# Kernel tuning notes

Measured on AMD Instinct MI355X. Metric: run time of the kernel, lower is better.

## Reference

```python
import jax, jax.numpy as jnp
import numpy as np

DIM = 1024
NUM_HEADS = 16
HEAD_DIM = DIM // NUM_HEADS


def setup_inputs() -> dict:
    key = jax.random.key(0)
    ks = jax.random.split(key, 9)
    B, T, D = 4, 8192, DIM
    s = 1.0 / np.sqrt(D)
    return {
        "x": jax.random.normal(ks[0], (B, T, D), dtype=jnp.float32),
        "Wq": jax.random.normal(ks[1], (D, D), dtype=jnp.float32) * s,
        "bq": jnp.zeros((D,), dtype=jnp.float32),
        "Wk": jax.random.normal(ks[2], (D, D), dtype=jnp.float32) * s,
        "bk": jnp.zeros((D,), dtype=jnp.float32),
        "Wv": jax.random.normal(ks[3], (D, D), dtype=jnp.float32) * s,
        "bv": jnp.zeros((D,), dtype=jnp.float32),
        "Wo": jax.random.normal(ks[4], (D, D), dtype=jnp.float32) * s,
        "bo": jnp.zeros((D,), dtype=jnp.float32),
    }


def _feature_map(x):
    # elu(x) + 1
    return jax.nn.elu(x) + 1.0


def reference(x, Wq, bq, Wk, bk, Wv, bv, Wo, bo):
    B, T, D = x.shape
    H, hd = NUM_HEADS, HEAD_DIM
    q = (x @ Wq.T + bq).reshape(B, T, H, hd)
    k = (x @ Wk.T + bk).reshape(B, T, H, hd)
    v = (x @ Wv.T + bv).reshape(B, T, H, hd)
    q = _feature_map(q)
    k = _feature_map(k)
    eps = 1e-6
    kv = jnp.einsum('bthd,bthm->bhmd', k, v)      # [B,H,hd,hd]
    k_sum = k.sum(axis=1)                          # [B,H,hd]
    z = 1.0 / (jnp.einsum('bthd,bhd->bth', q, k_sum) + eps)
    out = jnp.einsum('bthd,bhmd->bthm', q, kv) * z[..., None]
    out = out.reshape(B, T, D)
    return out @ Wo.T + bo
```

## Files before the change

kernel.cpp:

```cpp
#include <hip/hip_runtime.h>
#include <stdint.h>

typedef __bf16 bf16x8 __attribute__((ext_vector_type(8)));
typedef float f32x4 __attribute__((ext_vector_type(4)));
typedef unsigned short u16x8 __attribute__((ext_vector_type(8)));
typedef unsigned short u16x4 __attribute__((ext_vector_type(4)));

#define MFMA16(a, b, c) __builtin_amdgcn_mfma_f32_16x16x32_bf16(a, b, c, 0, 0, 0)

#define TSEQ 8192
#define BATCH 4
#define MROWS (BATCH * TSEQ)

static __device__ __forceinline__ unsigned short f2bf(float f) {
  union { float f; unsigned u; } v; v.f = f;
  unsigned u = v.u + 0x7FFFu + ((v.u >> 16) & 1u);
  return (unsigned short)(u >> 16);
}
static __device__ __forceinline__ float bf2f(unsigned short h) {
  union { unsigned u; float f; } v; v.u = ((unsigned)h) << 16; return v.f;
}
static __device__ __forceinline__ void gload16(const void* g, void* l) {
  __builtin_amdgcn_global_load_lds((const __attribute__((address_space(1))) void*)g,
                                   (__attribute__((address_space(3))) void*)l, 16, 0, 0);
}

__global__ __launch_bounds__(256) void cvt_bf16(const float* __restrict__ s,
                                                unsigned short* __restrict__ d, int n) {
  int i = (blockIdx.x * 256 + threadIdx.x) * 8;
  if (i >= n) return;
  const float4 a = *(const float4*)(s + i);
  const float4 b = *(const float4*)(s + i + 4);
  u16x8 o;
  o[0] = f2bf(a.x); o[1] = f2bf(a.y); o[2] = f2bf(a.z); o[3] = f2bf(a.w);
  o[4] = f2bf(b.x); o[5] = f2bf(b.y); o[6] = f2bf(b.z); o[7] = f2bf(b.w);
  *(u16x8*)(d + i) = o;
}

static __device__ __forceinline__ void gemm_core(const unsigned short* __restrict__ A,
                                                 const unsigned short* __restrict__ B,
                                                 int rowA0, int rowB0,
                                                 char* As, char* Bs, f32x4 acc[4][4]) {
  const int tid = threadIdx.x;
  const int l = tid & 63, w = tid >> 6;
  const int wr = (w >> 1) * 64, wc = (w & 1) * 64;
  for (int kk = 0; kk < 1024; kk += 32) {
    #pragma unroll
    for (int r2 = 0; r2 < 2; ++r2) {
      const int ci = r2 * 256 + tid;
      const int row = ci >> 2;
      const int csrc = (ci & 3) ^ ((row >> 1) & 3);
      char* la = As + (r2 * 256 + w * 64) * 16;
      gload16(A + (size_t)(rowA0 + row) * 1024 + kk + csrc * 8, la);
      char* lb = Bs + (r2 * 256 + w * 64) * 16;
      gload16(B + (size_t)(rowB0 + row) * 1024 + kk + csrc * 8, lb);
    }
    __syncthreads();
    bf16x8 af[4], bfr[4];
    #pragma unroll
    for (int m = 0; m < 4; ++m) {
      const int r = wr + m * 16 + (l & 15);
      const int c = (l >> 4) ^ ((r >> 1) & 3);
      af[m] = *(const bf16x8*)(As + r * 64 + c * 16);
      const int rb = wc + m * 16 + (l & 15);
      const int cb = (l >> 4) ^ ((rb >> 1) & 3);
      bfr[m] = *(const bf16x8*)(Bs + rb * 64 + cb * 16);
    }
    #pragma unroll
    for (int m = 0; m < 4; ++m)
      #pragma unroll
      for (int n = 0; n < 4; ++n)
        acc[m][n] = MFMA16(af[m], bfr[n], acc[m][n]);
    __syncthreads();
  }
}

__global__ __launch_bounds__(256) void qkv_gemm(const unsigned short* __restrict__ xbf,
                                                const unsigned short* __restrict__ wcat,
                                                const float* __restrict__ bq,
                                                const float* __restrict__ bk,
                                                const float* __restrict__ bv,
                                                unsigned short* __restrict__ qout,
                                                unsigned short* __restrict__ kout,
                                                unsigned short* __restrict__ vout) {
  __shared__ char As[8192];
  __shared__ char Bs[8192];
  f32x4 acc[4][4] = {};
  const int bx = blockIdx.x, by = blockIdx.y;
  gemm_core(xbf, wcat, by * 128, bx * 128, As, Bs, acc);

  const int region = bx >> 3;
  const float* bias = (region == 0) ? bq : (region == 1) ? bk : bv;
  unsigned short* dst = (region == 0) ? qout : (region == 1) ? kout : vout;
  const int l = threadIdx.x & 63, w = threadIdx.x >> 6;
  const int wr = (w >> 1) * 64, wc = (w & 1) * 64;
  const int colbase = (bx & 7) * 128 + wc;
  #pragma unroll
  for (int m = 0; m < 4; ++m) {
    #pragma unroll
    for (int n = 0; n < 4; ++n) {
      const int col = colbase + n * 16 + (l & 15);
      const float bb = bias[col];
      #pragma unroll
      for (int j = 0; j < 4; ++j) {
        const int row = by * 128 + wr + m * 16 + (l >> 4) * 4 + j;
        float v = acc[m][n][j] + bb;
        if (region < 2) v = (v > 0.f) ? (v + 1.f) : __expf(v);
        dst[(size_t)row * 1024 + col] = f2bf(v);
      }
    }
  }
}

__global__ __launch_bounds__(64) void kv_reduce(const unsigned short* __restrict__ kbf,
                                                const unsigned short* __restrict__ vbf,
                                                float* __restrict__ part) {
  const int bh = blockIdx.x, tc = blockIdx.y;
  const int b = bh >> 4, h = bh & 15;
  const int l = threadIdx.x;
  const int tm = l & 15, td = l >> 4;
  const unsigned short* kb = kbf + (size_t)b * TSEQ * 1024 + h * 64;
  const unsigned short* vb = vbf + (size_t)b * TSEQ * 1024 + h * 64;
  float acc[4][16] = {};
  float ksum = 0.f;
  const int t0 = tc * 256;
  #pragma unroll 2
  for (int t = t0; t < t0 + 256; ++t) {
    const unsigned short* krow = kb + (size_t)t * 1024;
    const unsigned short* vrow = vb + (size_t)t * 1024;
    const u16x8 k8a = *(const u16x8*)(krow + td * 16);
    const u16x8 k8b = *(const u16x8*)(krow + td * 16 + 8);
    const u16x4 v4 = *(const u16x4*)(vrow + tm * 4);
    float kf[16];
    #pragma unroll
    for (int j = 0; j < 8; ++j) { kf[j] = bf2f(k8a[j]); kf[8 + j] = bf2f(k8b[j]); }
    float vf[4];
    #pragma unroll
    for (int i = 0; i < 4; ++i) vf[i] = bf2f(v4[i]);
    ksum += bf2f(krow[td * 16 + tm]);
    #pragma unroll
    for (int i = 0; i < 4; ++i)
      #pragma unroll
      for (int j = 0; j < 16; ++j)
        acc[i][j] += vf[i] * kf[j];
  }
  float* ps = part + (size_t)(tc * 64 + bh) * 65 * 64;
  #pragma unroll
  for (int i = 0; i < 4; ++i) {
    const int m = tm * 4 + i;
    #pragma unroll
    for (int j = 0; j < 16; j += 4) {
      float4 o = make_float4(acc[i][j], acc[i][j + 1], acc[i][j + 2], acc[i][j + 3]);
      *(float4*)(ps + m * 64 + td * 16 + j) = o;
    }
  }
  ps[64 * 64 + td * 16 + tm] = ksum;
}

__global__ __launch_bounds__(256) void kv_finalize(const float* __restrict__ part,
                                                   unsigned short* __restrict__ bmat) {
  const int e = blockIdx.x * 256 + threadIdx.x;
  if (e >= 64 * 80 * 64) return;
  const int d = e & 63;
  const int r = (e >> 6) % 80;
  const int bh = e / (80 * 64);
  float s = 0.f;
  if (r < 65) {
    #pragma unroll
    for (int tc = 0; tc < 32; ++tc)
      s += part[((size_t)(tc * 64 + bh) * 65 + r) * 64 + d];
  }
  bmat[e] = f2bf(s);
}

__global__ __launch_bounds__(256) void attn_gemm(const unsigned short* __restrict__ qbf,
                                                 const unsigned short* __restrict__ bmat,
                                                 unsigned short* __restrict__ attn) {
  __shared__ char Qs[16384];
  __shared__ char Bs2[10240];
  const int bh = blockIdx.x, mt = blockIdx.y;
  const int b = bh >> 4, h = bh & 15;
  const int tid = threadIdx.x, l = tid & 63, w = tid >> 6;

  const unsigned short* qbase = qbf + (size_t)(b * TSEQ + mt * 128) * 1024 + h * 64;
  #pragma unroll
  for (int r4 = 0; r4 < 4; ++r4) {
    const int ci = r4 * 256 + tid;
    const int row = ci >> 3;
    const int csrc = (ci & 7) ^ (row & 7);
    gload16(qbase + (size_t)row * 1024 + csrc * 8, Qs + (r4 * 256 + w * 64) * 16);
  }
  const unsigned short* bbase = bmat + (size_t)bh * 80 * 64;
  #pragma unroll
  for (int r4 = 0; r4 < 3; ++r4) {
    const int ci = r4 * 256 + tid;
    if (ci < 640) {
      const int row = ci >> 3;
      const int csrc = (ci & 7) ^ (row & 7);
      gload16(bbase + row * 64 + csrc * 8, Bs2 + (r4 * 256 + w * 64) * 16);
    }
  }
  __syncthreads();

  f32x4 acc[2][5] = {};
  #pragma unroll
  for (int ks = 0; ks < 2; ++ks) {
    bf16x8 af[2], bfr[5];
    #pragma unroll
    for (int m = 0; m < 2; ++m) {
      const int r = w * 32 + m * 16 + (l & 15);
      const int c = ((l >> 4) + ks * 4) ^ (r & 7);
      af[m] = *(const bf16x8*)(Qs + r * 128 + c * 16);
    }
    #pragma unroll
    for (int n = 0; n < 5; ++n) {
      const int r = n * 16 + (l & 15);
      const int c = ((l >> 4) + ks * 4) ^ (r & 7);
      bfr[n] = *(const bf16x8*)(Bs2 + r * 128 + c * 16);
    }
    #pragma unroll
    for (int m = 0; m < 2; ++m)
      #pragma unroll
      for (int n = 0; n < 5; ++n)
        acc[m][n] = MFMA16(af[m], bfr[n], acc[m][n]);
  }

  unsigned short* arow = attn + (size_t)(b * TSEQ + mt * 128) * 1024 + h * 64;
  #pragma unroll
  for (int m = 0; m < 2; ++m) {
    #pragma unroll
    for (int j = 0; j < 4; ++j) {
      const float den = __shfl(acc[m][4][j], (l & 48));
      const float z = 1.f / (den + 1e-6f);
      const int row = w * 32 + m * 16 + (l >> 4) * 4 + j;
      #pragma unroll
      for (int n = 0; n < 4; ++n)
        arow[(size_t)row * 1024 + n * 16 + (l & 15)] = f2bf(acc[m][n][j] * z);
    }
  }
}

__global__ __launch_bounds__(256) void o_gemm(const unsigned short* __restrict__ attn,
                                              const unsigned short* __restrict__ wo,
                                              const float* __restrict__ bo,
                                              float* __restrict__ out) {
  __shared__ char As[8192];
  __shared__ char Bs[8192];
  f32x4 acc[4][4] = {};
  const int bx = blockIdx.x, by = blockIdx.y;
  gemm_core(attn, wo, by * 128, bx * 128, As, Bs, acc);
  const int l = threadIdx.x & 63, w = threadIdx.x >> 6;
  const int wr = (w >> 1) * 64, wc = (w & 1) * 64;
  #pragma unroll
  for (int m = 0; m < 4; ++m) {
    #pragma unroll
    for (int n = 0; n < 4; ++n) {
      const int col = bx * 128 + wc + n * 16 + (l & 15);
      const float bb = bo[col];
      #pragma unroll
      for (int j = 0; j < 4; ++j) {
        const int row = by * 128 + wr + m * 16 + (l >> 4) * 4 + j;
        out[(size_t)row * 1024 + col] = acc[m][n][j] + bb;
      }
    }
  }
}

extern "C" void kernel_launch(void* const* d_in, const int* in_sizes, int n_in,
                              void* d_out, int out_size, void* d_ws, size_t ws_size,
                              hipStream_t stream) {
  const float* x  = (const float*)d_in[0];
  const float* Wq = (const float*)d_in[1];
  const float* bq = (const float*)d_in[2];
  const float* Wk = (const float*)d_in[3];
  const float* bk = (const float*)d_in[4];
  const float* Wv = (const float*)d_in[5];
  const float* bv = (const float*)d_in[6];
  const float* Wo = (const float*)d_in[7];
  const float* bo = (const float*)d_in[8];
  float* out = (float*)d_out;
  char* ws = (char*)d_ws;

  unsigned short* xbf  = (unsigned short*)(ws + 0);
  unsigned short* wcat = (unsigned short*)(ws + 67108864);
  unsigned short* wobf = (unsigned short*)(ws + 73400320);
  unsigned short* qbf  = (unsigned short*)(ws + 75497472);
  unsigned short* kbf  = (unsigned short*)(ws + 142606336);
  unsigned short* vbf  = (unsigned short*)(ws + 209715200);
  float* part          = (float*)(ws + 0);
  unsigned short* bmat = (unsigned short*)(ws + 34078720);
  unsigned short* attn = kbf;

  cvt_bf16<<<16384, 256, 0, stream>>>(x, xbf, 33554432);
  cvt_bf16<<<512, 256, 0, stream>>>(Wq, wcat, 1048576);
  cvt_bf16<<<512, 256, 0, stream>>>(Wk, wcat + 1048576, 1048576);
  cvt_bf16<<<512, 256, 0, stream>>>(Wv, wcat + 2097152, 1048576);
  cvt_bf16<<<512, 256, 0, stream>>>(Wo, wobf, 1048576);

  qkv_gemm<<<dim3(24, 256), 256, 0, stream>>>(xbf, wcat, bq, bk, bv, qbf, kbf, vbf);
  kv_reduce<<<dim3(64, 32), 64, 0, stream>>>(kbf, vbf, part);
  kv_finalize<<<1280, 256, 0, stream>>>(part, bmat);
  attn_gemm<<<dim3(64, 64), 256, 0, stream>>>(qbf, bmat, attn);
  o_gemm<<<dim3(8, 256), 256, 0, stream>>>(attn, wobf, bo, out);
}
```

Measured before the change: 766.8 us.

## Replace QKV and output GEMMs with 256x256-tile pipelined 8-wave kernels

Both large projection GEMMs move from 128x128 tiles with a single-buffered LDS loop to 256x256 tiles on 512 threads. The new loop double-buffers A and B in LDS, issues global-to-LDS loads for the next k-slice while MFMAs run, and uses explicit waitcnt, barriers and setprio to interleave loads with compute. A swizzled block order improves L2 reuse across tiles. The larger tiles raise arithmetic intensity per byte loaded, at the cost of more registers and LDS per block, and the hand-written wait/barrier schedule is easy to get subtly wrong.

```diff
diff --git a/kernel.cpp b/kernel.cpp
--- a/kernel.cpp
+++ b/kernel.cpp
@@ -7,10 +7,14 @@
 typedef unsigned short u16x4 __attribute__((ext_vector_type(4)));
 
 #define MFMA16(a, b, c) __builtin_amdgcn_mfma_f32_16x16x32_bf16(a, b, c, 0, 0, 0)
+#define BAR() __builtin_amdgcn_s_barrier()
+#define LGK0() do { asm volatile("s_waitcnt lgkmcnt(0)" ::: "memory"); \
+                    __builtin_amdgcn_sched_barrier(0); } while (0)
+#define VMC(n) asm volatile("s_waitcnt vmcnt(" #n ")" ::: "memory")
+#define PRIO(p) __builtin_amdgcn_s_setprio(p)
 
 #define TSEQ 8192
 #define BATCH 4
-#define MROWS (BATCH * TSEQ)
 
 static __device__ __forceinline__ unsigned short f2bf(float f) {
   union { float f; unsigned u; } v; v.f = f;
@@ -37,76 +41,177 @@
   *(u16x8*)(d + i) = o;
 }
 
-static __device__ __forceinline__ void gemm_core(const unsigned short* __restrict__ A,
-                                                 const unsigned short* __restrict__ B,
-                                                 int rowA0, int rowB0,
-                                                 char* As, char* Bs, f32x4 acc[4][4]) {
-  const int tid = threadIdx.x;
-  const int l = tid & 63, w = tid >> 6;
-  const int wr = (w >> 1) * 64, wc = (w & 1) * 64;
-  for (int kk = 0; kk < 1024; kk += 32) {
-    #pragma unroll
-    for (int r2 = 0; r2 < 2; ++r2) {
-      const int ci = r2 * 256 + tid;
-      const int row = ci >> 2;
-      const int csrc = (ci & 3) ^ ((row >> 1) & 3);
-      char* la = As + (r2 * 256 + w * 64) * 16;
-      gload16(A + (size_t)(rowA0 + row) * 1024 + kk + csrc * 8, la);
-      char* lb = Bs + (r2 * 256 + w * 64) * 16;
-      gload16(B + (size_t)(rowB0 + row) * 1024 + kk + csrc * 8, lb);
-    }
-    __syncthreads();
-    bf16x8 af[4], bfr[4];
-    #pragma unroll
-    for (int m = 0; m < 4; ++m) {
-      const int r = wr + m * 16 + (l & 15);
-      const int c = (l >> 4) ^ ((r >> 1) & 3);
-      af[m] = *(const bf16x8*)(As + r * 64 + c * 16);
-      const int rb = wc + m * 16 + (l & 15);
-      const int cb = (l >> 4) ^ ((rb >> 1) & 3);
-      bfr[m] = *(const bf16x8*)(Bs + rb * 64 + cb * 16);
-    }
-    #pragma unroll
-    for (int m = 0; m < 4; ++m)
-      #pragma unroll
-      for (int n = 0; n < 4; ++n)
-        acc[m][n] = MFMA16(af[m], bfr[n], acc[m][n]);
-    __syncthreads();
-  }
-}
-
-__global__ __launch_bounds__(256) void qkv_gemm(const unsigned short* __restrict__ xbf,
-                                                const unsigned short* __restrict__ wcat,
-                                                const float* __restrict__ bq,
-                                                const float* __restrict__ bk,
-                                                const float* __restrict__ bv,
-                                                unsigned short* __restrict__ qout,
-                                                unsigned short* __restrict__ kout,
-                                                unsigned short* __restrict__ vout) {
-  __shared__ char As[8192];
-  __shared__ char Bs[8192];
-  f32x4 acc[4][4] = {};
-  const int bx = blockIdx.x, by = blockIdx.y;
-  gemm_core(xbf, wcat, by * 128, bx * 128, As, Bs, acc);
-
-  const int region = bx >> 3;
+
+static __device__ __forceinline__ void stage_ht(const unsigned short* __restrict__ G,
+                                                int grow0, char* Lbase, int t, int h,
+                                                int tid, int w) {
+  const int prow = tid >> 2, cp = tid & 3;
+  const int gch = cp ^ ((prow >> 1) & 3);
+  const unsigned short* src = G + (size_t)(grow0 + h * 128 + prow) * 1024 + t * 32 + gch * 8;
+  char* dst = Lbase + (t & 1) * 16384 + h * 8192 + w * 1024;
+  gload16(src, dst);
+}
+
+static __device__ __forceinline__ void mfma_quad(f32x4 acc[8][4], const bf16x8* a,
+                                                 const bf16x8* b, int m0) {
+  #pragma unroll
+  for (int mf = 0; mf < 4; ++mf)
+    #pragma unroll
+    for (int nf = 0; nf < 4; ++nf)
+      acc[m0 + mf][nf] = MFMA16(a[m0 + mf], b[nf], acc[m0 + mf][nf]);
+}
+
+static __device__ __forceinline__ void gemm256(const unsigned short* __restrict__ A,
+                                               const unsigned short* __restrict__ B,
+                                               int rowA0, int rowB0,
+                                               char* As, char* Bs, f32x4 acc[8][4]) {
+  const int tid = threadIdx.x, l = tid & 63, w = tid >> 6;
+  const int wr = w >> 2, wc = w & 3;
+  int a_off[8], b_off[4];
+  #pragma unroll
+  for (int mf = 0; mf < 8; ++mf) {
+    const int r = wr * 128 + mf * 16 + (l & 15);
+    const int cp = (l >> 4) ^ ((r >> 1) & 3);
+    a_off[mf] = r * 64 + cp * 16;
+  }
+  #pragma unroll
+  for (int nf = 0; nf < 4; ++nf) {
+    const int r = wc * 64 + nf * 16 + (l & 15);
+    const int cp = (l >> 4) ^ ((r >> 1) & 3);
+    b_off[nf] = r * 64 + cp * 16;
+  }
+  stage_ht(A, rowA0, As, 0, 0, tid, w);
+  stage_ht(A, rowA0, As, 0, 1, tid, w);
+  stage_ht(B, rowB0, Bs, 0, 0, tid, w);
+  stage_ht(B, rowB0, Bs, 0, 1, tid, w);
+  stage_ht(A, rowA0, As, 1, 0, tid, w);
+  stage_ht(A, rowA0, As, 1, 1, tid, w);
+  VMC(2);
+  BAR();
+
+  #pragma unroll 1
+  for (int i = 0; i < 15; ++i) {
+    const int t1 = 2 * i + 1;
+    bf16x8 a0[8], b0[4];
+    #pragma unroll
+    for (int mf = 0; mf < 8; ++mf) a0[mf] = *(const bf16x8*)(As + a_off[mf]);
+    #pragma unroll
+    for (int nf = 0; nf < 4; ++nf) b0[nf] = *(const bf16x8*)(Bs + b_off[nf]);
+    stage_ht(B, rowB0, Bs, t1, 0, tid, w);
+    stage_ht(B, rowB0, Bs, t1, 1, tid, w);
+    BAR(); LGK0(); PRIO(1);
+    mfma_quad(acc, a0, b0, 0);
+    PRIO(0); BAR();
+    stage_ht(A, rowA0, As, t1 + 1, 0, tid, w);
+    stage_ht(A, rowA0, As, t1 + 1, 1, tid, w);
+    BAR(); PRIO(1);
+    mfma_quad(acc, a0, b0, 4);
+    PRIO(0);
+    VMC(2);
+    BAR();
+    bf16x8 a1[8], b1[4];
+    #pragma unroll
+    for (int mf = 0; mf < 8; ++mf) a1[mf] = *(const bf16x8*)(As + 16384 + a_off[mf]);
+    #pragma unroll
+    for (int nf = 0; nf < 4; ++nf) b1[nf] = *(const bf16x8*)(Bs + 16384 + b_off[nf]);
+    stage_ht(B, rowB0, Bs, t1 + 1, 0, tid, w);
+    stage_ht(B, rowB0, Bs, t1 + 1, 1, tid, w);
+    BAR(); LGK0(); PRIO(1);
+    mfma_quad(acc, a1, b1, 0);
+    PRIO(0); BAR();
+    stage_ht(A, rowA0, As, t1 + 2, 0, tid, w);
+    stage_ht(A, rowA0, As, t1 + 2, 1, tid, w);
+    BAR(); PRIO(1);
+    mfma_quad(acc, a1, b1, 4);
+    PRIO(0);
+    VMC(2);
+    BAR();
+  }
+  {
+    bf16x8 a0[8], b0[4];
+    #pragma unroll
+    for (int mf = 0; mf < 8; ++mf) a0[mf] = *(const bf16x8*)(As + a_off[mf]);
+    #pragma unroll
+    for (int nf = 0; nf < 4; ++nf) b0[nf] = *(const bf16x8*)(Bs + b_off[nf]);
+    stage_ht(B, rowB0, Bs, 31, 0, tid, w);
+    stage_ht(B, rowB0, Bs, 31, 1, tid, w);
+    BAR(); LGK0(); PRIO(1);
+    mfma_quad(acc, a0, b0, 0);
+    PRIO(0); BAR();
+    PRIO(1);
+    mfma_quad(acc, a0, b0, 4);
+    PRIO(0);
+    VMC(0);
+    BAR();
+    bf16x8 a1[8], b1[4];
+    #pragma unroll
+    for (int mf = 0; mf < 8; ++mf) a1[mf] = *(const bf16x8*)(As + 16384 + a_off[mf]);
+    #pragma unroll
+    for (int nf = 0; nf < 4; ++nf) b1[nf] = *(const bf16x8*)(Bs + 16384 + b_off[nf]);
+    LGK0(); PRIO(1);
+    mfma_quad(acc, a1, b1, 0);
+    mfma_quad(acc, a1, b1, 4);
+    PRIO(0);
+  }
+}
+
+__global__ __launch_bounds__(512, 2) void qkv_gemm256(
+    const unsigned short* __restrict__ xbf, const unsigned short* __restrict__ wcat,
+    const float* __restrict__ bq, const float* __restrict__ bk, const float* __restrict__ bv,
+    unsigned short* __restrict__ qout, unsigned short* __restrict__ kout,
+    unsigned short* __restrict__ vout) {
+  __shared__ char As[32768];
+  __shared__ char Bs[32768];
+  const int swz = (blockIdx.x & 7) * 192 + (blockIdx.x >> 3);
+  const int mt = swz / 12, nt = swz % 12;
+  f32x4 acc[8][4] = {};
+  gemm256(xbf, wcat, mt * 256, nt * 256, As, Bs, acc);
+
+  const int l = threadIdx.x & 63, w = threadIdx.x >> 6;
+  const int wr = w >> 2, wc = w & 3;
+  const int region = nt >> 2;
   const float* bias = (region == 0) ? bq : (region == 1) ? bk : bv;
   unsigned short* dst = (region == 0) ? qout : (region == 1) ? kout : vout;
-  const int l = threadIdx.x & 63, w = threadIdx.x >> 6;
-  const int wr = (w >> 1) * 64, wc = (w & 1) * 64;
-  const int colbase = (bx & 7) * 128 + wc;
-  #pragma unroll
-  for (int m = 0; m < 4; ++m) {
-    #pragma unroll
-    for (int n = 0; n < 4; ++n) {
-      const int col = colbase + n * 16 + (l & 15);
+  const int colb = (nt & 3) * 256 + wc * 64;
+  #pragma unroll
+  for (int mf = 0; mf < 8; ++mf) {
+    #pragma unroll
+    for (int nf = 0; nf < 4; ++nf) {
+      const int col = colb + nf * 16 + (l & 15);
       const float bb = bias[col];
       #pragma unroll
       for (int j = 0; j < 4; ++j) {
-        const int row = by * 128 + wr + m * 16 + (l >> 4) * 4 + j;
-        float v = acc[m][n][j] + bb;
+        const int row = mt * 256 + wr * 128 + mf * 16 + (l >> 4) * 4 + j;
+        float v = acc[mf][nf][j] + bb;
         if (region < 2) v = (v > 0.f) ? (v + 1.f) : __expf(v);
         dst[(size_t)row * 1024 + col] = f2bf(v);
+      }
+    }
+  }
+}
+
+__global__ __launch_bounds__(512, 2) void o_gemm256(
+    const unsigned short* __restrict__ attn, const unsigned short* __restrict__ wo,
+    const float* __restrict__ bo, float* __restrict__ out) {
+  __shared__ char As[32768];
+  __shared__ char Bs[32768];
+  const int swz = (blockIdx.x & 7) * 64 + (blockIdx.x >> 3);
+  const int mt = swz >> 2, nt = swz & 3;
+  f32x4 acc[8][4] = {};
+  gemm256(attn, wo, mt * 256, nt * 256, As, Bs, acc);
+
+  const int l = threadIdx.x & 63, w = threadIdx.x >> 6;
+  const int wr = w >> 2, wc = w & 3;
+  #pragma unroll
+  for (int mf = 0; mf < 8; ++mf) {
+    #pragma unroll
+    for (int nf = 0; nf < 4; ++nf) {
+      const int col = nt * 256 + wc * 64 + nf * 16 + (l & 15);
+      const float bb = bo[col];
+      #pragma unroll
+      for (int j = 0; j < 4; ++j) {
+        const int row = mt * 256 + wr * 128 + mf * 16 + (l >> 4) * 4 + j;
+        out[(size_t)row * 1024 + col] = acc[mf][nf][j] + bb;
       }
     }
   }
@@ -240,32 +345,6 @@
   }
 }
 
-__global__ __launch_bounds__(256) void o_gemm(const unsigned short* __restrict__ attn,
-                                              const unsigned short* __restrict__ wo,
-                                              const float* __restrict__ bo,
-                                              float* __restrict__ out) {
-  __shared__ char As[8192];
-  __shared__ char Bs[8192];
-  f32x4 acc[4][4] = {};
-  const int bx = blockIdx.x, by = blockIdx.y;
-  gemm_core(attn, wo, by * 128, bx * 128, As, Bs, acc);
-  const int l = threadIdx.x & 63, w = threadIdx.x >> 6;
-  const int wr = (w >> 1) * 64, wc = (w & 1) * 64;
-  #pragma unroll
-  for (int m = 0; m < 4; ++m) {
-    #pragma unroll
-    for (int n = 0; n < 4; ++n) {
-      const int col = bx * 128 + wc + n * 16 + (l & 15);
-      const float bb = bo[col];
-      #pragma unroll
-      for (int j = 0; j < 4; ++j) {
-        const int row = by * 128 + wr + m * 16 + (l >> 4) * 4 + j;
-        out[(size_t)row * 1024 + col] = acc[m][n][j] + bb;
-      }
-    }
-  }
-}
-
 extern "C" void kernel_launch(void* const* d_in, const int* in_sizes, int n_in,
                               void* d_out, int out_size, void* d_ws, size_t ws_size,
                               hipStream_t stream) {
@@ -297,9 +376,9 @@
   cvt_bf16<<<512, 256, 0, stream>>>(Wv, wcat + 2097152, 1048576);
   cvt_bf16<<<512, 256, 0, stream>>>(Wo, wobf, 1048576);
 
-  qkv_gemm<<<dim3(24, 256), 256, 0, stream>>>(xbf, wcat, bq, bk, bv, qbf, kbf, vbf);
+  qkv_gemm256<<<1536, 512, 0, stream>>>(xbf, wcat, bq, bk, bv, qbf, kbf, vbf);
   kv_reduce<<<dim3(64, 32), 64, 0, stream>>>(kbf, vbf, part);
   kv_finalize<<<1280, 256, 0, stream>>>(part, bmat);
   attn_gemm<<<dim3(64, 64), 256, 0, stream>>>(qbf, bmat, attn);
-  o_gemm<<<dim3(8, 256), 256, 0, stream>>>(attn, wobf, bo, out);
-}
+  o_gemm256<<<512, 512, 0, stream>>>(attn, wobf, bo, out);
+}
```

Measured after the change: 699.1 us. 8.8% less time.
